# Kernel tuning notes

Measured on AMD Instinct MI355X. Metric: run time of the kernel, lower is better.

Reference implementation:

```python
import jax, jax.numpy as jnp
import numpy as np

ALPHA = 2000.0
TAU = 1e-07
K = 3
TOL = 1e-06
MAX_ITER = 50
T = 1048576  # 2**20
EPS = 1e-08


def setup_inputs() -> dict:
    key = jax.random.key(0)
    k1, k2 = jax.random.split(key)
    x = jax.random.normal(k1, (T,), dtype=jnp.float32)
    omega0 = jax.random.uniform(k2, (K,), dtype=jnp.float32)  # torch does 0.5*rand(K); scaled in reference
    return {"x": x, "omega0": omega0}


def _vmd(x, omega0):
    Tn = x.shape[0]
    freqs = jnp.arange(1, Tn + 1, dtype=jnp.float32) / Tn - 0.5 - 1.0 / Tn  # [T]
    f_hat = jnp.fft.fftshift(jnp.fft.fft(x.astype(jnp.complex64)))  # [T] complex64
    omega = 0.5 * omega0  # init == 1
    u0 = jnp.zeros((K, Tn), dtype=jnp.complex64)
    lam0 = jnp.zeros((Tn,), dtype=jnp.complex64)

    def step(carry, n):
        u_out, u_prev, lam_prev, om, done = carry
        # --- u_hat update (vectorized over k; torch k-loop uses stale omega) ---
        d_self = (freqs[None, :] - om[:, None]) ** 2            # [K,T]
        denom = d_self + TAU ** 2
        denom = denom.at[1:].add(d_self[:-1])                    # + (freqs - omega[k-1])^2 for k>0
        denom = denom.at[:-1].add(d_self[1:])                    # + (freqs - omega[k+1])^2 for k<K-1
        u_new = (f_hat[None, :] - lam_prev[None, :] / 2) / (1.0 + ALPHA * denom)  # [K,T]
        # --- omega update (DC == 0 branch) ---
        power = jnp.abs(u_new) ** 2                              # [K,T] float32
        om_new = jnp.sum(power * freqs[None, :], axis=1) / (jnp.sum(power, axis=1) + EPS)
        # --- dual ascent ---
        lam_new = lam_prev + TAU * (jnp.sum(u_new, axis=0) - f_hat)
        # --- convergence check every 10 outer iterations (torch break -> done flag) ---
        u_diff = jnp.sum(jnp.abs(u_new - u_prev) ** 2) / (jnp.sum(jnp.abs(u_prev) ** 2) + EPS)
        o_diff = jnp.sum(jnp.abs(om_new - jnp.roll(om_new, 1))) / K
        conv = (n % 10 == 0) & (u_diff < TOL) & (o_diff < TOL)
        new = (u_new, u_new, lam_new, om_new, done | conv)
        old = (u_out, u_prev, lam_prev, om, done)
        out = jax.tree_util.tree_map(lambda a, b: jnp.where(done, a, b), old, new)
        return out, None

    carry = (u0, u0, lam0, omega, jnp.array(False))
    (u_final, _, _, _, _), _ = jax.lax.scan(step, carry, jnp.arange(MAX_ITER))
    imfs = jnp.fft.ifft(jnp.fft.ifftshift(u_final, axes=1), axis=1).real.astype(x.dtype)  # [K,T]
    return imfs


def reference(x, omega0):
    return _vmd(x, omega0)
```

## Files before the change

kernel.cpp:

```cpp
#include <hip/hip_runtime.h>
#include <math.h>


#define TN        (1 << 20)
#define NBINS     1024
#define PPB       1024
#define FALPHA    2000.0f
#define FTAU      1e-7f
#define FTOL      1e-6f
#define FEPS      1e-8f
#define FTWO_PI   6.28318530717958647692f
#define FINV_T    (1.0f / 1048576.0f)

__device__ __forceinline__ float2 cmulf(float2 a, float2 b) {
    return make_float2(a.x * b.x - a.y * b.y, a.x * b.y + a.y * b.x);
}
__device__ __forceinline__ float2 cisf(float a) {
    float s, c;
    __sincosf(a, &s, &c);
    return make_float2(c, s);
}
__device__ __forceinline__ float rlanef(float v, int l) {
    return __int_as_float(__builtin_amdgcn_readlane(__float_as_int(v), l));
}

__device__ __forceinline__ void g3f(float fr, float om0, float om1, float om2,
                                    float& g0, float& g1, float& g2) {
    const float tau2 = FTAU * FTAU;
    float d0 = fr - om0; d0 *= d0;
    float d1 = fr - om1; d1 *= d1;
    float d2 = fr - om2; d2 *= d2;
    g0 = __builtin_amdgcn_rcpf(1.0f + FALPHA * (d0 + d1 + tau2));
    g1 = __builtin_amdgcn_rcpf(1.0f + FALPHA * (d0 + d1 + d2 + tau2));
    g2 = __builtin_amdgcn_rcpf(1.0f + FALPHA * (d1 + d2 + tau2));
}

__device__ __forceinline__ float dpp_wave_sum(float x) {
    x += __int_as_float(__builtin_amdgcn_update_dpp(
             0, __float_as_int(x), 0x111, 0xf, 0xf, true));
    x += __int_as_float(__builtin_amdgcn_update_dpp(
             0, __float_as_int(x), 0x112, 0xf, 0xf, true));
    x += __int_as_float(__builtin_amdgcn_update_dpp(
             0, __float_as_int(x), 0x114, 0xf, 0xf, true));
    x += __int_as_float(__builtin_amdgcn_update_dpp(
             0, __float_as_int(x), 0x118, 0xf, 0xf, true));
    x += __int_as_float(__builtin_amdgcn_update_dpp(
             0, __float_as_int(x), 0x142, 0xf, 0xf, true));
    x += __int_as_float(__builtin_amdgcn_update_dpp(
             0, __float_as_int(x), 0x143, 0xf, 0xf, true));
    return x;
}
__device__ __forceinline__ float dpp_sum32(float x) {
    x += __int_as_float(__builtin_amdgcn_update_dpp(
             0, __float_as_int(x), 0x111, 0xf, 0xf, true));
    x += __int_as_float(__builtin_amdgcn_update_dpp(
             0, __float_as_int(x), 0x112, 0xf, 0xf, true));
    x += __int_as_float(__builtin_amdgcn_update_dpp(
             0, __float_as_int(x), 0x114, 0xf, 0xf, true));
    x += __int_as_float(__builtin_amdgcn_update_dpp(
             0, __float_as_int(x), 0x118, 0xf, 0xf, true));
    x += __int_as_float(__builtin_amdgcn_update_dpp(
             0, __float_as_int(x), 0x142, 0xf, 0xf, true));
    return x;
}

__global__ __launch_bounds__(256)
void k_binpart(const float2* __restrict__ in, float* __restrict__ pB,
               float* __restrict__ pM) {
    __shared__ float tile[32][33];
    const int bx = blockIdx.x * 32, by = blockIdx.y * 32;
    const int tx = threadIdx.x, ty = threadIdx.y;
#pragma unroll
    for (int j = 0; j < 32; j += 8) {
        const float2 v = in[(size_t)(by + ty + j) * 1024 + bx + tx];
        tile[ty + j][tx] = v.x * v.x + v.y * v.y;
    }
    __syncthreads();
    const int sIdx = blockIdx.y;
    const float d = ((float)(by + tx) - 511.5f) * FINV_T;
    const int lane = (tx + 32 * ty) & 63;
#pragma unroll
    for (int j = 0; j < 32; j += 8) {
        float s = tile[tx][ty + j];
        float m = s * d;
        s = dpp_sum32(s);
        m = dpp_sum32(m);
        if (lane == 31 || lane == 63) {
            const int bin = bx + ty + j;
            pB[bin * 32 + sIdx] = s;
            pM[bin * 32 + sIdx] = m;
        }
    }
}

__global__ __launch_bounds__(512)
void k_omega(const float* __restrict__ pB, const float* __restrict__ pM,
             const float* __restrict__ omega0,
             float* __restrict__ oomf, float* __restrict__ sgsb) {
    const int tid = threadIdx.x;
    const int lane = tid & 63, wid = tid >> 6;
    const float kA = -4.0f * FALPHA;

    float B[2], M[2], C[2], SG[2], gp[2];
#pragma unroll
    for (int i = 0; i < 2; ++i) {
        const int j = tid + 512 * i;
        float sb = 0.f, sm = 0.f;
#pragma unroll
        for (int s = 0; s < 32; ++s) {
            sb += pB[j * 32 + s];
            sm += pM[j * 32 + s];
        }
        B[i] = sb; M[i] = sm;
        C[i] = ((float)(j * PPB) + 511.5f) * FINV_T - 0.5f;
        SG[i] = 0.f; gp[i] = 0.f;
    }

    float om0 = 0.5f * omega0[0];
    float om1 = 0.5f * omega0[1];
    float om2 = 0.5f * omega0[2];
    float op0 = om0, op1 = om1, op2 = om2;
    float n0 = om0, n1 = om1, n2 = om2;
    float stop = 0.f;

    __shared__ float wsum[2][8][8];
    bool fin = true;

    for (int n = 0; n < 49; ++n) {
        if (n > 0) {
            if (stop != 0.f) { fin = false; break; }
            op0 = om0; op1 = om1; op2 = om2;
            om0 = n0; om1 = n1; om2 = n2;
#pragma unroll
            for (int i = 0; i < 2; ++i) SG[i] += gp[i] - 1.0f;
        }
        const int check = (n > 0 && n % 10 == 0);

        float a[8];
#pragma unroll
        for (int v = 0; v < 8; ++v) a[v] = 0.f;

#pragma unroll
        for (int i = 0; i < 2; ++i) {
            const float c  = C[i];
            const float Bv = B[i];
            const float M1 = M[i];
            const float e0 = c - om0, e1 = c - om1, e2 = c - om2;
            float g0, g1, g2;
            g3f(c, om0, om1, om2, g0, g1, g2);
            const float gsq0 = g0 * g0, gsq1 = g1 * g1, gsq2 = g2 * g2;
            const float gc0 = gsq0 * g0, gc1 = gsq1 * g1, gc2 = gsq2 * g2;
            const float Dp0 = e0 + e1, Dp1 = e0 + e1 + e2, Dp2 = e1 + e2;
            const float P0 = gsq0 * Bv + kA * Dp0 * gc0 * M1;
            const float P1 = gsq1 * Bv + kA * Dp1 * gc1 * M1;
            const float P2 = gsq2 * Bv + kA * Dp2 * gc2 * M1;
            a[0] += P0; a[1] += P1; a[2] += P2;
            a[3] += c * P0 + gsq0 * M1;
            a[4] += c * P1 + gsq1 * M1;
            a[5] += c * P2 + gsq2 * M1;
            gp[i] = g0 + g1 + g2;
            if (check) {
                float h0, h1, h2;
                g3f(c, op0, op1, op2, h0, h1, h2);
                const float d0 = g0 - h0, d1 = g1 - h1, d2 = g2 - h2;
                a[6] += Bv * (d0 * d0 + d1 * d1 + d2 * d2);
                a[7] += Bv * (h0 * h0 + h1 * h1 + h2 * h2);
            }
        }
#pragma unroll
        for (int v = 0; v < 8; ++v) a[v] = dpp_wave_sum(a[v]);
        if (lane == 63) {
            *(float4*)&wsum[n & 1][wid][0] = make_float4(a[0], a[1], a[2], a[3]);
            *(float4*)&wsum[n & 1][wid][4] = make_float4(a[4], a[5], a[6], a[7]);
        }
        __syncthreads();
        float r = 0.f;
#pragma unroll
        for (int w = 0; w < 8; ++w) r += wsum[n & 1][w][lane & 7];
        const float S0 = rlanef(r, 0), S1 = rlanef(r, 1), S2 = rlanef(r, 2);
        const float S3 = rlanef(r, 3), S4 = rlanef(r, 4), S5 = rlanef(r, 5);
        n0 = S3 * __builtin_amdgcn_rcpf(S0 + FEPS);
        n1 = S4 * __builtin_amdgcn_rcpf(S1 + FEPS);
        n2 = S5 * __builtin_amdgcn_rcpf(S2 + FEPS);
        if (check) {
            const float S6 = rlanef(r, 6), S7 = rlanef(r, 7);
            const float ud = S6 * __builtin_amdgcn_rcpf(S7 + FEPS);
            const float od = (fabsf(n0 - n2) + fabsf(n1 - n0) +
                              fabsf(n2 - n1)) * (1.0f / 3.0f);
            stop = (ud < FTOL && od < FTOL) ? 1.f : 0.f;
        }
    }

    if (fin) {
#pragma unroll
        for (int i = 0; i < 2; ++i) SG[i] += gp[i] - 1.0f;
        om0 = n0; om1 = n1; om2 = n2;
    }
#pragma unroll
    for (int i = 0; i < 2; ++i) sgsb[tid + 512 * i] = SG[i];
    if (tid == 0) { oomf[0] = om0; oomf[1] = om1; oomf[2] = om2; }
}

__device__ __forceinline__ float2* fft1024_stages(float2* bufA, float2* bufB,
                                                  int t, float dir) {
    float2* src = bufA;
    float2* dst = bufB;
    int Ns = 1;
#pragma unroll
    for (int s = 0; s < 5; ++s) {
        const int jm = t & (Ns - 1);
        float2 v0 = src[t], v1 = src[t + 256], v2 = src[t + 512], v3 = src[t + 768];
        const float a = dir * (FTWO_PI * 0.25f) * ((float)jm / (float)Ns);
        float2 w1 = cisf(a);
        float2 w2 = cmulf(w1, w1);
        float2 w3 = cmulf(w2, w1);
        v1 = cmulf(v1, w1); v2 = cmulf(v2, w2); v3 = cmulf(v3, w3);
        float2 s0 = make_float2(v0.x + v2.x, v0.y + v2.y);
        float2 s1 = make_float2(v0.x - v2.x, v0.y - v2.y);
        float2 s2 = make_float2(v1.x + v3.x, v1.y + v3.y);
        float2 s3 = make_float2(v1.x - v3.x, v1.y - v3.y);
        float2 s3i = make_float2(-dir * s3.y, dir * s3.x);
        const int base = ((t - jm) << 2) + jm;
        dst[base]          = make_float2(s0.x + s2.x, s0.y + s2.y);
        dst[base + Ns]     = make_float2(s1.x + s3i.x, s1.y + s3i.y);
        dst[base + 2 * Ns] = make_float2(s0.x - s2.x, s0.y - s2.y);
        dst[base + 3 * Ns] = make_float2(s1.x - s3i.x, s1.y - s3i.y);
        __syncthreads();
        float2* tmp = src; src = dst; dst = tmp;
        Ns <<= 2;
    }
    return src;
}

__global__ __launch_bounds__(256)
void k_fft1024(const float2* __restrict__ in, float2* __restrict__ out,
               float dir, int do_tw) {
    __shared__ float2 bufA[1024];
    __shared__ float2 bufB[1024];
    const int row  = blockIdx.x;
    const int rowm = row & 1023;
    const float2* __restrict__ rin  = in  + (size_t)row * 1024;
    float2* __restrict__ rout = out + (size_t)row * 1024;
    const int t = threadIdx.x;
#pragma unroll
    for (int r = 0; r < 4; ++r) bufA[t + 256 * r] = rin[t + 256 * r];
    __syncthreads();
    float2* src = fft1024_stages(bufA, bufB, t, dir);
#pragma unroll
    for (int r = 0; r < 4; ++r) {
        const int c = t + 256 * r;
        float2 xv = src[c];
        if (do_tw) {
            const unsigned p = ((unsigned)rowm * (unsigned)c) & 1048575u;
            xv = cmulf(xv, cisf(dir * (FTWO_PI * FINV_T) * (float)p));
        }
        rout[c] = xv;
    }
}

__global__ __launch_bounds__(256)
void k_fftu(const float2* __restrict__ fhat, const float* __restrict__ sgsb,
            const float* __restrict__ oomf,
            float2* __restrict__ out, int zbase) {
    __shared__ float2 bufA[1024];
    __shared__ float2 bufB[1024];
    const int row = blockIdx.x & 1023;
    const int zi  = blockIdx.x >> 10;
    const int z   = zi + zbase;
    const float om0 = oomf[0], om1 = oomf[1], om2 = oomf[2];
    const float2* __restrict__ frow = fhat + (size_t)row * 1024;
    const int t = threadIdx.x;
#pragma unroll
    for (int r = 0; r < 4; ++r) {
        const int c = t + 256 * r;
        const float2 f = frow[c];
        const int tt = (c << 10) | row;
        const float fr = (float)tt * FINV_T - 0.5f;
        const float sc = 1.0f - 0.5f * FTAU * sgsb[tt >> 10];
        float g0, g1, g2;
        g3f(fr, om0, om1, om2, g0, g1, g2);
        const int tm = (TN - tt) & (TN - 1);
        const float frm = (float)tm * FINV_T - 0.5f;
        const float scm = 1.0f - 0.5f * FTAU * sgsb[tm >> 10];
        float h0, h1, h2;
        g3f(frm, om0, om1, om2, h0, h1, h2);
        float A, Bi;
        if (z == 0) {
            A  = 0.5f * (g0 * sc + h0 * scm);
            Bi = 0.5f * (g1 * sc + h1 * scm);
        } else {
            A  = 0.5f * (g2 * sc + h2 * scm);
            Bi = 0.f;
        }
        bufA[c] = cmulf(f, make_float2(A, Bi));
    }
    __syncthreads();
    float2* src = fft1024_stages(bufA, bufB, t, 1.0f);
    float2* __restrict__ rout = out + (size_t)zi * TN + (size_t)row * 1024;
#pragma unroll
    for (int r = 0; r < 4; ++r) {
        const int c = t + 256 * r;
        const unsigned p = ((unsigned)row * (unsigned)c) & 1048575u;
        rout[c] = cmulf(src[c], cisf((FTWO_PI * FINV_T) * (float)p));
    }
}

__global__ __launch_bounds__(256)
void k_tr_c2c(const float2* __restrict__ in, float2* __restrict__ out) {
    __shared__ float2 tile[32][33];
    const size_t zo = (size_t)blockIdx.z * TN;
    const int bx = blockIdx.x * 32, by = blockIdx.y * 32;
    const int tx = threadIdx.x, ty = threadIdx.y;
#pragma unroll
    for (int j = 0; j < 32; j += 8)
        tile[ty + j][tx] = in[zo + (size_t)(by + ty + j) * 1024 + bx + tx];
    __syncthreads();
#pragma unroll
    for (int j = 0; j < 32; j += 8)
        out[zo + (size_t)(bx + ty + j) * 1024 + by + tx] = tile[tx][ty + j];
}

__global__ __launch_bounds__(256)
void k_tr_fwd_in(const float* __restrict__ in, float2* __restrict__ out) {
    __shared__ float tile[32][33];
    const int bx = blockIdx.x * 32, by = blockIdx.y * 32;
    const int tx = threadIdx.x, ty = threadIdx.y;
#pragma unroll
    for (int j = 0; j < 32; j += 8)
        tile[ty + j][tx] = in[(size_t)(by + ty + j) * 1024 + bx + tx];
    __syncthreads();
#pragma unroll
    for (int j = 0; j < 32; j += 8) {
        const int r = bx + ty + j;
        float v = tile[tx][ty + j];
        v = (r & 1) ? -v : v;
        out[(size_t)r * 1024 + by + tx] = make_float2(v, 0.0f);
    }
}

__global__ __launch_bounds__(256)
void k_tr_out(const float2* __restrict__ in, float* __restrict__ out,
              int zbase) {
    __shared__ float2 tile[32][33];
    const int z = blockIdx.z + zbase;
    const size_t zo = (size_t)blockIdx.z * TN;
    const int bx = blockIdx.x * 32, by = blockIdx.y * 32;
    const int tx = threadIdx.x, ty = threadIdx.y;
#pragma unroll
    for (int j = 0; j < 32; j += 8)
        tile[ty + j][tx] = in[zo + (size_t)(by + ty + j) * 1024 + bx + tx];
    __syncthreads();
    const int c = by + tx;
    const float sgn = (c & 1) ? -FINV_T : FINV_T;
#pragma unroll
    for (int j = 0; j < 32; j += 8) {
        const int r = bx + ty + j;
        const float2 v = tile[tx][ty + j];
        const size_t idx = (size_t)r * 1024 + c;
        if (z == 0) {
            out[idx]              = v.x * sgn;
            out[(size_t)TN + idx] = v.y * sgn;
        } else {
            out[2 * (size_t)TN + idx] = v.x * sgn;
        }
    }
}

extern "C" void kernel_launch(void* const* d_in, const int* in_sizes, int n_in,
                              void* d_out, int out_size, void* d_ws, size_t ws_size,
                              hipStream_t stream) {
    (void)in_sizes; (void)n_in; (void)out_size;
    const float* x      = (const float*)d_in[0];
    const float* omega0 = (const float*)d_in[1];
    float* outp = (float*)d_out;
    char* ws = (char*)d_ws;

    const size_t MB = (size_t)1 << 20;
    const size_t KB = (size_t)1 << 10;
    float2* fhat = (float2*)(ws);
    float*  pB   = (float*)(ws + 8 * MB);
    float*  pM   = (float*)(ws + 8 * MB + 128 * KB);
    float*  sgsb = (float*)(ws + 8 * MB + 256 * KB);
    float*  oomf = (float*)(ws + 8 * MB + 264 * KB);
    const bool batch2 = ws_size >= 42 * MB;
    float2* sA = (float2*)(ws + 9 * MB);
    float2* sB = batch2 ? (float2*)(ws + 25 * MB)
                        : (float2*)(ws + 17 * MB);

    dim3 tb(32, 8);
    dim3 tg(32, 32);

    k_tr_fwd_in<<<tg, tb, 0, stream>>>(x, sA);
    k_fft1024<<<1024, 256, 0, stream>>>(sA, sB, -1.0f, 1);
    k_tr_c2c<<<tg, tb, 0, stream>>>(sB, sA);
    k_fft1024<<<1024, 256, 0, stream>>>(sA, fhat, -1.0f, 0);

    k_binpart<<<tg, tb, 0, stream>>>(fhat, pB, pM);

    k_omega<<<1, 512, 0, stream>>>(pB, pM, omega0, oomf, sgsb);

    if (batch2) {
        k_fftu<<<2048, 256, 0, stream>>>(fhat, sgsb, oomf, sB, 0);
        k_tr_c2c<<<dim3(32, 32, 2), tb, 0, stream>>>(sB, sA);
        k_fft1024<<<2048, 256, 0, stream>>>(sA, sB, 1.0f, 0);
        k_tr_out<<<dim3(32, 32, 2), tb, 0, stream>>>(sB, outp, 0);
    } else {
        for (int z = 0; z < 2; ++z) {
            k_fftu<<<1024, 256, 0, stream>>>(fhat, sgsb, oomf, sB, z);
            k_tr_c2c<<<tg, tb, 0, stream>>>(sB, sA);
            k_fft1024<<<1024, 256, 0, stream>>>(sA, sB, 1.0f, 0);
            k_tr_out<<<dim3(32, 32, 1), tb, 0, stream>>>(sB, outp, z);
        }
    }
}
```

Measured before the change: 180.5 us.

## Run omega iteration kernel as a single wavefront without block barriers

The serial omega-update kernel now runs as one 64-lane wavefront, each lane handling 16 bins instead of 2. The per-iteration shared-memory exchange and __syncthreads are replaced by DPP wave reductions and readlane. The convergence-check sums are reduced only on check iterations, kA*M is precomputed, and partials load as float4. Each iteration does 8x more serial work per lane but drops 49 block barriers and LDS round trips, which could cost more on a latency-bound single-CU kernel.

```diff
diff --git a/kernel.cpp b/kernel.cpp
--- a/kernel.cpp
+++ b/kernel.cpp
@@ -93,25 +93,26 @@
     }
 }
 
-__global__ __launch_bounds__(512)
-void k_omega(const float* __restrict__ pB, const float* __restrict__ pM,
+__global__ __launch_bounds__(64)
+void k_omega(const float4* __restrict__ pB4, const float4* __restrict__ pM4,
              const float* __restrict__ omega0,
              float* __restrict__ oomf, float* __restrict__ sgsb) {
-    const int tid = threadIdx.x;
-    const int lane = tid & 63, wid = tid >> 6;
+    const int lane = threadIdx.x;
     const float kA = -4.0f * FALPHA;
 
-    float B[2], M[2], C[2], SG[2], gp[2];
-#pragma unroll
-    for (int i = 0; i < 2; ++i) {
-        const int j = tid + 512 * i;
+    float B[16], M[16], KM[16], C[16], SG[16], gp[16];
+#pragma unroll
+    for (int i = 0; i < 16; ++i) {
+        const int j = lane + 64 * i;
         float sb = 0.f, sm = 0.f;
 #pragma unroll
-        for (int s = 0; s < 32; ++s) {
-            sb += pB[j * 32 + s];
-            sm += pM[j * 32 + s];
-        }
-        B[i] = sb; M[i] = sm;
+        for (int s = 0; s < 8; ++s) {
+            const float4 b4 = pB4[j * 8 + s];
+            const float4 m4 = pM4[j * 8 + s];
+            sb += b4.x + b4.y + b4.z + b4.w;
+            sm += m4.x + m4.y + m4.z + m4.w;
+        }
+        B[i] = sb; M[i] = sm; KM[i] = kA * sm;
         C[i] = ((float)(j * PPB) + 511.5f) * FINV_T - 0.5f;
         SG[i] = 0.f; gp[i] = 0.f;
     }
@@ -122,8 +123,6 @@
     float op0 = om0, op1 = om1, op2 = om2;
     float n0 = om0, n1 = om1, n2 = om2;
     float stop = 0.f;
-
-    __shared__ float wsum[2][8][8];
     bool fin = true;
 
     for (int n = 0; n < 49; ++n) {
@@ -132,7 +131,7 @@
             op0 = om0; op1 = om1; op2 = om2;
             om0 = n0; om1 = n1; om2 = n2;
 #pragma unroll
-            for (int i = 0; i < 2; ++i) SG[i] += gp[i] - 1.0f;
+            for (int i = 0; i < 16; ++i) SG[i] += gp[i] - 1.0f;
         }
         const int check = (n > 0 && n % 10 == 0);
 
@@ -141,9 +140,10 @@
         for (int v = 0; v < 8; ++v) a[v] = 0.f;
 
 #pragma unroll
-        for (int i = 0; i < 2; ++i) {
+        for (int i = 0; i < 16; ++i) {
             const float c  = C[i];
             const float Bv = B[i];
+            const float KMv = KM[i];
             const float M1 = M[i];
             const float e0 = c - om0, e1 = c - om1, e2 = c - om2;
             float g0, g1, g2;
@@ -151,9 +151,9 @@
             const float gsq0 = g0 * g0, gsq1 = g1 * g1, gsq2 = g2 * g2;
             const float gc0 = gsq0 * g0, gc1 = gsq1 * g1, gc2 = gsq2 * g2;
             const float Dp0 = e0 + e1, Dp1 = e0 + e1 + e2, Dp2 = e1 + e2;
-            const float P0 = gsq0 * Bv + kA * Dp0 * gc0 * M1;
-            const float P1 = gsq1 * Bv + kA * Dp1 * gc1 * M1;
-            const float P2 = gsq2 * Bv + kA * Dp2 * gc2 * M1;
+            const float P0 = gsq0 * Bv + Dp0 * gc0 * KMv;
+            const float P1 = gsq1 * Bv + Dp1 * gc1 * KMv;
+            const float P2 = gsq2 * Bv + Dp2 * gc2 * KMv;
             a[0] += P0; a[1] += P1; a[2] += P2;
             a[3] += c * P0 + gsq0 * M1;
             a[4] += c * P1 + gsq1 * M1;
@@ -168,22 +168,17 @@
             }
         }
 #pragma unroll
-        for (int v = 0; v < 8; ++v) a[v] = dpp_wave_sum(a[v]);
-        if (lane == 63) {
-            *(float4*)&wsum[n & 1][wid][0] = make_float4(a[0], a[1], a[2], a[3]);
-            *(float4*)&wsum[n & 1][wid][4] = make_float4(a[4], a[5], a[6], a[7]);
-        }
-        __syncthreads();
-        float r = 0.f;
-#pragma unroll
-        for (int w = 0; w < 8; ++w) r += wsum[n & 1][w][lane & 7];
-        const float S0 = rlanef(r, 0), S1 = rlanef(r, 1), S2 = rlanef(r, 2);
-        const float S3 = rlanef(r, 3), S4 = rlanef(r, 4), S5 = rlanef(r, 5);
+        for (int v = 0; v < 6; ++v) a[v] = dpp_wave_sum(a[v]);
+        const float S0 = rlanef(a[0], 63), S1 = rlanef(a[1], 63);
+        const float S2 = rlanef(a[2], 63), S3 = rlanef(a[3], 63);
+        const float S4 = rlanef(a[4], 63), S5 = rlanef(a[5], 63);
         n0 = S3 * __builtin_amdgcn_rcpf(S0 + FEPS);
         n1 = S4 * __builtin_amdgcn_rcpf(S1 + FEPS);
         n2 = S5 * __builtin_amdgcn_rcpf(S2 + FEPS);
         if (check) {
-            const float S6 = rlanef(r, 6), S7 = rlanef(r, 7);
+            a[6] = dpp_wave_sum(a[6]);
+            a[7] = dpp_wave_sum(a[7]);
+            const float S6 = rlanef(a[6], 63), S7 = rlanef(a[7], 63);
             const float ud = S6 * __builtin_amdgcn_rcpf(S7 + FEPS);
             const float od = (fabsf(n0 - n2) + fabsf(n1 - n0) +
                               fabsf(n2 - n1)) * (1.0f / 3.0f);
@@ -193,12 +188,12 @@
 
     if (fin) {
 #pragma unroll
-        for (int i = 0; i < 2; ++i) SG[i] += gp[i] - 1.0f;
+        for (int i = 0; i < 16; ++i) SG[i] += gp[i] - 1.0f;
         om0 = n0; om1 = n1; om2 = n2;
     }
 #pragma unroll
-    for (int i = 0; i < 2; ++i) sgsb[tid + 512 * i] = SG[i];
-    if (tid == 0) { oomf[0] = om0; oomf[1] = om1; oomf[2] = om2; }
+    for (int i = 0; i < 16; ++i) sgsb[lane + 64 * i] = SG[i];
+    if (lane == 0) { oomf[0] = om0; oomf[1] = om1; oomf[2] = om2; }
 }
 
 __device__ __forceinline__ float2* fft1024_stages(float2* bufA, float2* bufB,
@@ -397,7 +392,8 @@
 
     k_binpart<<<tg, tb, 0, stream>>>(fhat, pB, pM);
 
-    k_omega<<<1, 512, 0, stream>>>(pB, pM, omega0, oomf, sgsb);
+    k_omega<<<1, 64, 0, stream>>>((const float4*)pB, (const float4*)pM,
+                                  omega0, oomf, sgsb);
 
     if (batch2) {
         k_fftu<<<2048, 256, 0, stream>>>(fhat, sgsb, oomf, sB, 0);
```

Result: slower. 229.5 us (+27.1%).
